# Kernel optimization log

Hardware: AMD Instinct MI355X
Metric: run time of the kernel (lower is better)

## Reference

```python
import jax, jax.numpy as jnp
import numpy as np

D, D_SEQ, D_HEAD, N_HEAD = 256, 1280, 48, 8
N_NODE, B_GRAPH, S_LEN = 2048, 8, 1024
HDH = N_HEAD * D_HEAD  # 384
SCALE = float(np.sqrt(D_HEAD))
LN_EPS = 1e-5


def setup_inputs() -> dict:
    key = jax.random.key(0)
    ks = jax.random.split(key, 12)
    node = jax.random.normal(ks[0], (N_NODE, D), dtype=jnp.float32)
    emb = jax.random.normal(ks[1], (B_GRAPH, S_LEN, D_SEQ), dtype=jnp.float32)
    mask = jax.random.randint(ks[2], (B_GRAPH, S_LEN), 0, 2, dtype=jnp.int32)
    batch = jnp.sort(jax.random.randint(ks[3], (N_NODE,), 0, B_GRAPH, dtype=jnp.int64))
    def lin(k, fan_in, fan_out):
        lim = 1.0 / np.sqrt(fan_in)
        return jax.random.uniform(k, (fan_in, fan_out), jnp.float32, -lim, lim)
    return {
        "node": node,
        "packed_sequence_emb": emb,
        "packed_sequence_mask": mask,
        "batch": batch,
        "ln_g": jnp.ones((D,), jnp.float32),
        "ln_b": jnp.zeros((D,), jnp.float32),
        "Wq": lin(ks[4], D, HDH),
        "Wk": lin(ks[5], D_SEQ, HDH),
        "Wv": lin(ks[6], D_SEQ, HDH),
        "Wg": lin(ks[7], D, HDH),
        "bg": jnp.zeros((HDH,), jnp.float32),
        "Wback": lin(ks[8], HDH, D),
        "bback": jnp.zeros((D,), jnp.float32),
    }


def _layernorm(x, g, b):
    mu = jnp.mean(x, axis=-1, keepdims=True)
    var = jnp.mean(jnp.square(x - mu), axis=-1, keepdims=True)
    return (x - mu) * jax.lax.rsqrt(var + LN_EPS) * g + b


def reference(node, packed_sequence_emb, packed_sequence_mask, batch,
              ln_g, ln_b, Wq, Wk, Wv, Wg, bg, Wback, bback):
    N = node.shape[0]
    y = _layernorm(node, ln_g, ln_b)                                   # [N, D]
    q = (y @ Wq).reshape(N, N_HEAD, D_HEAD)                            # [N, H, Dh]
    k = (packed_sequence_emb @ Wk).reshape(B_GRAPH, S_LEN, N_HEAD, D_HEAD)
    v = (packed_sequence_emb @ Wv).reshape(B_GRAPH, S_LEN, N_HEAD, D_HEAD)

    # scores[n, s, h] = <q[n,h], k[batch[n], s, h]> / sqrt(Dh)
    scores_all = jnp.einsum('nhd,bshd->nbsh', q, k) / SCALE            # [N, B, S, H]
    scores = jnp.take_along_axis(
        scores_all, batch[:, None, None, None].astype(jnp.int32), axis=1
    )[:, 0]                                                            # [N, S, H]

    # masked softmax over sequence axis (dim=1), mask broadcast over heads
    mask_f = packed_sequence_mask[batch].astype(scores.dtype)[:, :, None]  # [N, S, 1]
    s_max = jnp.max(jnp.where(mask_f > 0, scores, -jnp.inf), axis=1, keepdims=True)
    e = jnp.exp(scores - s_max) * mask_f
    w = e / (jnp.sum(e, axis=1, keepdims=True) + 1e-9)                 # [N, S, H]

    # out[n,h,d] = sum_s w[n,s,h] * v[batch[n], s, h, d]
    feat_all = jnp.einsum('nsh,bshd->nbhd', w, v)                      # [N, B, H, Dh]
    feat = jnp.take_along_axis(
        feat_all, batch[:, None, None, None].astype(jnp.int32), axis=1
    )[:, 0]                                                            # [N, H, Dh]

    gate = jax.nn.sigmoid(y @ Wg + bg).reshape(N, N_HEAD, D_HEAD)
    new = (gate * feat).reshape(N, HDH) @ Wback + bback
    return node + new
```

## Files before the change

kernel.cpp:

```cpp
#include <hip/hip_runtime.h>
#include <hip/hip_bf16.h>
#include <math.h>

#define D 256
#define D_SEQ 1280
#define D_HEAD 48
#define N_HEAD 8
#define HDH 384
#define N_NODE 2048
#define B_GRAPH 8
#define S_LEN 1024
#define LN_EPS 1e-5f
#define QSCALE (0.14433756729740643f * 1.4426950408889634f)
#define KVN 768
#define QGN 768
#define QROWS (N_NODE + 16)
#define TPG 40
#define NWL (TPG * 8)
#define PAD_T 164864

typedef unsigned short u16;
typedef __attribute__((ext_vector_type(8))) short short8;
typedef __attribute__((ext_vector_type(4))) short short4v;
typedef __attribute__((ext_vector_type(4))) unsigned short ushort4v;
typedef __attribute__((ext_vector_type(4))) float floatx4;

__device__ __forceinline__ u16 f2bf(float f) {
    unsigned int x = __float_as_uint(f);
    x += 0x7fff + ((x >> 16) & 1);
    return (u16)(x >> 16);
}

__device__ __forceinline__ void load_lds16(const u16* g, u16* lds) {
    __builtin_amdgcn_global_load_lds(
        (const __attribute__((address_space(1))) unsigned int*)g,
        (__attribute__((address_space(3))) unsigned int*)lds, 16, 0, 0);
}

__global__ __launch_bounds__(256)
void prep(const float* __restrict__ emb, u16* __restrict__ embb,
          const float* __restrict__ node, const float* __restrict__ ln_g,
          const float* __restrict__ ln_b, u16* __restrict__ yb,
          const float* __restrict__ Wk, const float* __restrict__ Wv,
          const float* __restrict__ Wq, const float* __restrict__ Wg,
          const float* __restrict__ Wback,
          u16* __restrict__ WT, u16* __restrict__ WT2, u16* __restrict__ WbT,
          const int* __restrict__ batch, int* __restrict__ ranges,
          int* __restrict__ wl, u16* __restrict__ Kp, u16* __restrict__ Qb) {
    const int bx = blockIdx.x;
    if (bx < 5120) {
        const size_t i = ((size_t)bx * 256 + threadIdx.x) * 8;
        const float4 a = *(const float4*)&emb[i];
        const float4 b = *(const float4*)&emb[i + 4];
        union { u16 u[8]; int4 v; } p;
        p.u[0]=f2bf(a.x); p.u[1]=f2bf(a.y); p.u[2]=f2bf(a.z); p.u[3]=f2bf(a.w);
        p.u[4]=f2bf(b.x); p.u[5]=f2bf(b.y); p.u[6]=f2bf(b.z); p.u[7]=f2bf(b.w);
        *(int4*)&embb[i] = p.v;
        return;
    }
    if (bx < 7168) {
        const int n = bx - 5120, t = threadIdx.x;
        float x = node[n * D + t];
        float s = x, sq = x * x;
        #pragma unroll
        for (int o = 32; o > 0; o >>= 1) {
            s  += __shfl_down(s, o);
            sq += __shfl_down(sq, o);
        }
        __shared__ float ss[4], sqs[4];
        if ((t & 63) == 0) { ss[t >> 6] = s; sqs[t >> 6] = sq; }
        __syncthreads();
        float S  = ss[0] + ss[1] + ss[2] + ss[3];
        float SQ = sqs[0] + sqs[1] + sqs[2] + sqs[3];
        float mu  = S * (1.f / D);
        float var = SQ * (1.f / D) - mu * mu;
        float inv = rsqrtf(var + LN_EPS);
        yb[n * D + t] = f2bf((x - mu) * inv * ln_g[t] + ln_b[t]);
        return;
    }
    if (bx < 8416) {
        int u = bx - 7168;
        const float* W; u16* WTo; int K, kx, ny, Ncols;
        if (u < 480)      { W = Wk;    WTo = WT;                       K = D_SEQ; Ncols = HDH; kx = u % 40; ny = u / 40; }
        else if (u < 960) { u -= 480;  W = Wv; WTo = WT + (size_t)HDH * D_SEQ; K = D_SEQ; Ncols = HDH; kx = u % 40; ny = u / 40; }
        else if (u < 1056){ u -= 960;  W = Wq; WTo = WT2;              K = D;   Ncols = HDH; kx = u % 8;  ny = u / 8; }
        else if (u < 1152){ u -= 1056; W = Wg; WTo = WT2 + (size_t)HDH * D; K = D; Ncols = HDH; kx = u % 8; ny = u / 8; }
        else              { u -= 1152; W = Wback; WTo = WbT;           K = HDH; Ncols = D;   kx = u % 12; ny = u / 12; }
        const int k0 = kx * 32, n0 = ny * 32;
        __shared__ float tile[32][33];
        const int tx = threadIdx.x & 31, ty = threadIdx.x >> 5;
        #pragma unroll
        for (int i = 0; i < 32; i += 8)
            tile[ty + i][tx] = W[(size_t)(k0 + ty + i) * Ncols + n0 + tx];
        __syncthreads();
        #pragma unroll
        for (int i = 0; i < 32; i += 8)
            WTo[(size_t)(n0 + ty + i) * K + k0 + tx] = f2bf(tile[tx][ty + i]);
        return;
    }
    if (bx == 8416) {
        int t = threadIdx.x;
        if (t <= B_GRAPH) {
            int lo = 0, hi = N_NODE;
            while (lo < hi) {
                int mid = (lo + hi) >> 1;
                if (batch[mid] < t) lo = mid + 1; else hi = mid;
            }
            ranges[t] = lo;
        }
        __syncthreads();
        if (t < B_GRAPH) {
            const int s = ranges[t];
            const int ntile = (ranges[t + 1] - s + 15) >> 4;
            for (int i = 0; i < TPG; ++i)
                wl[i * 8 + t] = (i < ntile) ? ((t << 16) | (s + i * 16)) : -1;
        }
        return;
    }
    const int t = (bx - 8417) * 256 + threadIdx.x;
    const int4 z = {0, 0, 0, 0};
    if (t < 131072) {
        const int row = t >> 1, half = t & 1;
        *(int4*)&Kp[(size_t)row * 64 + 48 + half * 8] = z;
    } else if (t < 164096) {
        const int u = t - 131072;
        const int row = u >> 1, half = u & 1;
        *(int4*)&Qb[(size_t)row * 64 + 48 + half * 8] = z;
    } else {
        const int u = t - 164096;
        const int row = u / 6, c = u - row * 6;
        const int hh = row >> 4, m = 2048 + (row & 15);
        *(int4*)&Qb[((size_t)hh * QROWS + m) * 64 + c * 8] = z;
    }
}

__global__ __launch_bounds__(256)
void kvqg_gemm(const u16* __restrict__ A, const u16* __restrict__ WT,
               u16* __restrict__ Kp, u16* __restrict__ V4,
               const u16* __restrict__ Ab, const u16* __restrict__ WT2,
               const float* __restrict__ bg, u16* __restrict__ Qb,
               float* __restrict__ gate) {
    __shared__ __align__(16) u16 As[128 * 32];
    __shared__ __align__(16) u16 Bs[128 * 32];
    const int tid = threadIdx.x;
    const int lane = tid & 63, wave = tid >> 6;
    const int wm64 = (wave >> 1) * 64, wn64 = (wave & 1) * 64;
    const int lm = lane & 15, lq = lane >> 4;

    if (blockIdx.x < 384) {
        const int glin = blockIdx.x;
        const int xcd = glin & 7, rest = glin >> 3;
        const int m0 = (xcd + 8 * (rest / 6)) * 128;
        const int n0 = (rest % 6) * 128;

        floatx4 acc[4][4] = {};

        const int srow = lane >> 2, scol = (lane & 3) * 8;
        const u16* ag  = &A[(size_t)(m0 + wave * 16 + srow) * D_SEQ + scol];
        const u16* ag2 = ag + (size_t)64 * D_SEQ;
        const u16* bgp = &WT[(size_t)(n0 + wave * 16 + srow) * D_SEQ + scol];
        const u16* bg2 = bgp + (size_t)64 * D_SEQ;
        u16* asb  = &As[wave * 512];
        u16* asb2 = &As[2048 + wave * 512];
        u16* bsb  = &Bs[wave * 512];
        u16* bsb2 = &Bs[2048 + wave * 512];

        for (int k0 = 0; k0 < D_SEQ; k0 += 32) {
            __syncthreads();
            load_lds16(ag + k0, asb);
            load_lds16(ag2 + k0, asb2);
            load_lds16(bgp + k0, bsb);
            load_lds16(bg2 + k0, bsb2);
            __syncthreads();

            short8 af[4], bfr[4];
            #pragma unroll
            for (int i = 0; i < 4; ++i)
                af[i] = *(const short8*)&As[(wm64 + i * 16 + lm) * 32 + lq * 8];
            #pragma unroll
            for (int j = 0; j < 4; ++j)
                bfr[j] = *(const short8*)&Bs[(wn64 + j * 16 + lm) * 32 + lq * 8];
            #pragma unroll
            for (int i = 0; i < 4; ++i)
                #pragma unroll
                for (int j = 0; j < 4; ++j)
                    acc[i][j] = __builtin_amdgcn_mfma_f32_16x16x32_bf16(
                        af[i], bfr[j], acc[i][j], 0, 0, 0);
        }

        #pragma unroll
        for (int i = 0; i < 4; ++i) {
            const int mrow = m0 + wm64 + i * 16 + lq * 4;
            const int bb = mrow >> 10, s = mrow & 1023;
            #pragma unroll
            for (int j = 0; j < 4; ++j) {
                const int n = n0 + wn64 + j * 16 + lm;
                if (n < HDH) {
                    const int hh = n / 48, dd = n - hh * 48;
                    u16* kp = &Kp[(((size_t)(bb * N_HEAD + hh)) * S_LEN + s) * 64 + dd];
                    kp[0]   = f2bf(acc[i][j][0]);
                    kp[64]  = f2bf(acc[i][j][1]);
                    kp[128] = f2bf(acc[i][j][2]);
                    kp[192] = f2bf(acc[i][j][3]);
                } else {
                    const int nv = n - HDH;
                    const int hh = nv / 48, dd = nv - hh * 48;
                    ushort4v pk;
                    pk[0] = f2bf(acc[i][j][0]); pk[1] = f2bf(acc[i][j][1]);
                    pk[2] = f2bf(acc[i][j][2]); pk[3] = f2bf(acc[i][j][3]);
                    *(ushort4v*)&V4[(((size_t)(bb * N_HEAD + hh)) * (S_LEN / 4) + (s >> 2)) * 192 + dd * 4] = pk;
                }
            }
        }
        return;
    }

    {
        const int u = blockIdx.x - 384;
        const int m0 = (u / 6) * 128, n0 = (u % 6) * 128;

        floatx4 acc[4][4] = {};
        const int sr = tid >> 2;
        const int sc = (tid & 3) * 8;

        for (int k0 = 0; k0 < D; k0 += 32) {
            const int4 a0 = *(const int4*)&Ab[(size_t)(m0 + sr) * D + k0 + sc];
            const int4 a1 = *(const int4*)&Ab[(size_t)(m0 + sr + 64) * D + k0 + sc];
            const int4 b0 = *(const int4*)&WT2[(size_t)(n0 + sr) * D + k0 + sc];
            const int4 b1 = *(const int4*)&WT2[(size_t)(n0 + sr + 64) * D + k0 + sc];
            __syncthreads();
            *(int4*)&As[sr * 32 + sc] = a0;
            *(int4*)&As[(sr + 64) * 32 + sc] = a1;
            *(int4*)&Bs[sr * 32 + sc] = b0;
            *(int4*)&Bs[(sr + 64) * 32 + sc] = b1;
            __syncthreads();

            short8 af[4], bfr[4];
            #pragma unroll
            for (int i = 0; i < 4; ++i)
                af[i] = *(const short8*)&As[(wm64 + i * 16 + lm) * 32 + lq * 8];
            #pragma unroll
            for (int i = 0; i < 4; ++i)
                bfr[i] = *(const short8*)&Bs[(wn64 + i * 16 + lm) * 32 + lq * 8];
            #pragma unroll
            for (int i = 0; i < 4; ++i)
                #pragma unroll
                for (int j = 0; j < 4; ++j)
                    acc[i][j] = __builtin_amdgcn_mfma_f32_16x16x32_bf16(
                        af[i], bfr[j], acc[i][j], 0, 0, 0);
        }

        #pragma unroll
        for (int i = 0; i < 4; ++i) {
            const int mb = m0 + wm64 + i * 16 + lq * 4;
            #pragma unroll
            for (int j = 0; j < 4; ++j) {
                const int n = n0 + wn64 + j * 16 + lm;
                #pragma unroll
                for (int r = 0; r < 4; ++r) {
                    const int m = mb + r;
                    const float v = acc[i][j][r];
                    if (n < HDH) {
                        const int hh = n / 48, dd = n - hh * 48;
                        Qb[((size_t)hh * QROWS + m) * 64 + dd] = f2bf(v * QSCALE);
                    } else {
                        const int ng = n - HDH;
                        gate[(size_t)m * HDH + ng] = 1.f / (1.f + __expf(-(v + bg[ng])));
                    }
                }
            }
        }
    }
}

__global__ __launch_bounds__(256)
void back_gemm(const u16* __restrict__ Ab, const u16* __restrict__ Bt,
               const float* __restrict__ bias, const float* __restrict__ resid,
               float* __restrict__ C) {
    __shared__ __align__(16) u16 As[128 * 32];
    __shared__ __align__(16) u16 Bs[128 * 32];
    const int tid = threadIdx.x;
    const int lane = tid & 63, wave = tid >> 6;
    const int wm = (wave >> 1) * 64, wn = (wave & 1) * 64;
    const int m0 = blockIdx.y * 128, n0 = blockIdx.x * 128;
    const int lm = lane & 15, lq = lane >> 4;

    floatx4 acc[4][4] = {};
    const int sr = tid >> 2;
    const int sc = (tid & 3) * 8;

    for (int k0 = 0; k0 < HDH; k0 += 32) {
        const int4 a0 = *(const int4*)&Ab[(size_t)(m0 + sr) * HDH + k0 + sc];
        const int4 a1 = *(const int4*)&Ab[(size_t)(m0 + sr + 64) * HDH + k0 + sc];
        const int4 b0 = *(const int4*)&Bt[(size_t)(n0 + sr) * HDH + k0 + sc];
        const int4 b1 = *(const int4*)&Bt[(size_t)(n0 + sr + 64) * HDH + k0 + sc];
        __syncthreads();
        *(int4*)&As[sr * 32 + sc] = a0;
        *(int4*)&As[(sr + 64) * 32 + sc] = a1;
        *(int4*)&Bs[sr * 32 + sc] = b0;
        *(int4*)&Bs[(sr + 64) * 32 + sc] = b1;
        __syncthreads();

        short8 af[4], bfr[4];
        #pragma unroll
        for (int i = 0; i < 4; ++i)
            af[i] = *(const short8*)&As[(wm + i * 16 + lm) * 32 + lq * 8];
        #pragma unroll
        for (int i = 0; i < 4; ++i)
            bfr[i] = *(const short8*)&Bs[(wn + i * 16 + lm) * 32 + lq * 8];
        #pragma unroll
        for (int i = 0; i < 4; ++i)
            #pragma unroll
            for (int j = 0; j < 4; ++j)
                acc[i][j] = __builtin_amdgcn_mfma_f32_16x16x32_bf16(
                    af[i], bfr[j], acc[i][j], 0, 0, 0);
    }

    #pragma unroll
    for (int i = 0; i < 4; ++i) {
        const int mb = m0 + wm + i * 16 + lq * 4;
        #pragma unroll
        for (int j = 0; j < 4; ++j) {
            const int n = n0 + wn + j * 16 + lm;
            #pragma unroll
            for (int r = 0; r < 4; ++r) {
                const int m = mb + r;
                C[(size_t)m * D + n] = acc[i][j][r] + bias[n] + resid[(size_t)m * D + n];
            }
        }
    }
}

struct Pref {
    short8 k0, k1;
    int4 mv;
    short4v v0, v1, v2;
};

__device__ __forceinline__ Pref ldpref(const u16* kbase, const u16* vbase,
                                       const int* mrow, int s, int lm, int lq) {
    Pref p;
    const u16* kr = &kbase[(size_t)(s + lm) * 64];
    p.k0 = *(const short8*)&kr[lq * 8];
    p.k1 = *(const short8*)&kr[32 + lq * 8];
    p.mv = *(const int4*)&mrow[s + lq * 4];
    const size_t vo = (size_t)((s >> 2) + lq) * 192;
    p.v0 = *(const short4v*)&vbase[vo];
    p.v1 = *(const short4v*)&vbase[vo + 64];
    p.v2 = *(const short4v*)&vbase[vo + 128];
    return p;
}

__global__ __launch_bounds__(256)
void attn_mfma(const u16* __restrict__ Qb, const u16* __restrict__ Kp,
               const u16* __restrict__ V4, const int* __restrict__ mask,
               const int* __restrict__ ranges, const int* __restrict__ wl,
               float* __restrict__ Pacc, float* __restrict__ Pl) {
    const int e = wl[blockIdx.x];
    if (e < 0) return;
    const int b = e >> 16, n0 = e & 0xffff;
    const int h = blockIdx.y, sp = blockIdx.z;
    const int nend = ranges[b + 1];
    const int NT = min(16, nend - n0);

    const int tid = threadIdx.x;
    const int wave = tid >> 6, lane = tid & 63;
    const int lm = lane & 15, lq = lane >> 4;
    const int bh = b * N_HEAD + h;

    const u16* qrow = &Qb[((size_t)h * QROWS + n0 + lm) * 64];
    const short8 qf0 = *(const short8*)&qrow[lq * 8];
    const short8 qf1 = *(const short8*)&qrow[32 + lq * 8];

    const u16* kbase = &Kp[(size_t)bh * S_LEN * 64];
    const u16* vbase = &V4[(size_t)bh * (S_LEN / 4) * 192 + (size_t)lm * 4];
    const int* mrow = &mask[b * S_LEN];

    float l_i = 0.f;
    floatx4 acc0 = {}, acc1 = {}, acc2 = {};

    const int sbase = sp * 512 + wave * 128;
    Pref pf[2];
    pf[0] = ldpref(kbase, vbase, mrow, sbase, lm, lq);
    pf[1] = ldpref(kbase, vbase, mrow, sbase + 16, lm, lq);

    #pragma unroll
    for (int t = 0; t < 8; ++t) {
        const Pref cur = pf[t & 1];
        if (t < 6)
            pf[t & 1] = ldpref(kbase, vbase, mrow, sbase + (t + 2) * 16, lm, lq);

        floatx4 st = {};
        st = __builtin_amdgcn_mfma_f32_16x16x32_bf16(cur.k0, qf0, st, 0, 0, 0);
        st = __builtin_amdgcn_mfma_f32_16x16x32_bf16(cur.k1, qf1, st, 0, 0, 0);

        const float p0 = cur.mv.x > 0 ? exp2f(st[0]) : 0.f;
        const float p1 = cur.mv.y > 0 ? exp2f(st[1]) : 0.f;
        const float p2 = cur.mv.z > 0 ? exp2f(st[2]) : 0.f;
        const float p3 = cur.mv.w > 0 ? exp2f(st[3]) : 0.f;
        l_i += (p0 + p1) + (p2 + p3);

        union { __hip_bfloat162 h2[2]; short4v v; } pu;
        pu.h2[0] = __float22bfloat162_rn(make_float2(p0, p1));
        pu.h2[1] = __float22bfloat162_rn(make_float2(p2, p3));

        acc0 = __builtin_amdgcn_mfma_f32_16x16x16bf16_1k(cur.v0, pu.v, acc0, 0, 0, 0);
        acc1 = __builtin_amdgcn_mfma_f32_16x16x16bf16_1k(cur.v1, pu.v, acc1, 0, 0, 0);
        acc2 = __builtin_amdgcn_mfma_f32_16x16x16bf16_1k(cur.v2, pu.v, acc2, 0, 0, 0);
    }

    l_i += __shfl_xor(l_i, 16);
    l_i += __shfl_xor(l_i, 32);

    __shared__ float sl[4][64];
    __shared__ float sacc[4][3][4][64];
    sl[wave][lane] = l_i;
    #pragma unroll
    for (int r = 0; r < 4; ++r) {
        sacc[wave][0][r][lane] = acc0[r];
        sacc[wave][1][r][lane] = acc1[r];
        sacc[wave][2][r][lane] = acc2[r];
    }
    __syncthreads();
    if (wave < 3 && lm < NT) {
        const int dt = wave;
        const float L = sl[0][lane] + sl[1][lane] + sl[2][lane] + sl[3][lane];
        const size_t o = (size_t)(n0 + lm) * HDH + h * 48 + dt * 16 + lq * 4;
        float4 ov;
        ov.x = sacc[0][dt][0][lane] + sacc[1][dt][0][lane] +
               sacc[2][dt][0][lane] + sacc[3][dt][0][lane];
        ov.y = sacc[0][dt][1][lane] + sacc[1][dt][1][lane] +
               sacc[2][dt][1][lane] + sacc[3][dt][1][lane];
        ov.z = sacc[0][dt][2][lane] + sacc[1][dt][2][lane] +
               sacc[2][dt][2][lane] + sacc[3][dt][2][lane];
        ov.w = sacc[0][dt][3][lane] + sacc[1][dt][3][lane] +
               sacc[2][dt][3][lane] + sacc[3][dt][3][lane];
        *(float4*)&Pacc[(size_t)sp * N_NODE * HDH + o] = ov;
        if (wave == 0 && lq == 0)
            Pl[(size_t)sp * N_NODE * N_HEAD + (n0 + lm) * N_HEAD + h] = L;
    }
}

__global__ __launch_bounds__(256)
void fuse_kernel(const float* __restrict__ Pacc, const float* __restrict__ Pl,
                 const float* __restrict__ gate, u16* __restrict__ gfeatb) {
    const size_t i4 = ((size_t)blockIdx.x * 256 + threadIdx.x) * 4;
    const int nh = (int)(i4 / 48);
    const float4 a = *(const float4*)&Pacc[i4];
    const float4 c = *(const float4*)&Pacc[(size_t)N_NODE * HDH + i4];
    const float4 g = *(const float4*)&gate[i4];
    const float L = Pl[nh] + Pl[N_NODE * N_HEAD + nh];
    const float inv = 1.f / (L + 1e-9f);
    union { __hip_bfloat162 h2[2]; ushort4v v; } r2;
    r2.h2[0] = __float22bfloat162_rn(make_float2((a.x + c.x) * inv * g.x,
                                                 (a.y + c.y) * inv * g.y));
    r2.h2[1] = __float22bfloat162_rn(make_float2((a.z + c.z) * inv * g.z,
                                                 (a.w + c.w) * inv * g.w));
    *(ushort4v*)&gfeatb[i4] = r2.v;
}

extern "C" void kernel_launch(void* const* d_in, const int* in_sizes, int n_in,
                              void* d_out, int out_size, void* d_ws, size_t ws_size,
                              hipStream_t stream) {
    const float* node  = (const float*)d_in[0];
    const float* emb   = (const float*)d_in[1];
    const int*   mask  = (const int*)d_in[2];
    const int*   batch = (const int*)d_in[3];
    const float* ln_g  = (const float*)d_in[4];
    const float* ln_b  = (const float*)d_in[5];
    const float* Wq    = (const float*)d_in[6];
    const float* Wk    = (const float*)d_in[7];
    const float* Wv    = (const float*)d_in[8];
    const float* Wg    = (const float*)d_in[9];
    const float* bg    = (const float*)d_in[10];
    const float* Wback = (const float*)d_in[11];
    const float* bback = (const float*)d_in[12];
    float* out = (float*)d_out;

    float* ws    = (float*)d_ws;
    float* gate  = ws;
    float* Pacc  = gate + (size_t)N_NODE * HDH;
    float* Pl    = Pacc + (size_t)2 * N_NODE * HDH;
    u16*   gfeatb = (u16*)(Pl + (size_t)2 * N_NODE * N_HEAD);
    u16*   yb    = gfeatb + (size_t)N_NODE * HDH;
    u16*   WT    = yb + (size_t)N_NODE * D;
    u16*   WT2   = WT + (size_t)KVN * D_SEQ;
    u16*   WbT   = WT2 + (size_t)QGN * D;
    u16*   Qb    = WbT + (size_t)D * HDH;
    u16*   Kp    = Qb + (size_t)N_HEAD * QROWS * 64;
    u16*   V4    = Kp + (size_t)B_GRAPH * N_HEAD * S_LEN * 64;
    u16*   embb  = V4 + (size_t)B_GRAPH * N_HEAD * (S_LEN / 4) * 192;
    int*   ranges = (int*)(embb + (size_t)B_GRAPH * S_LEN * D_SEQ);
    int*   wl    = ranges + 16;

    prep<<<8417 + PAD_T / 256, 256, 0, stream>>>(
        emb, embb, node, ln_g, ln_b, yb, Wk, Wv, Wq, Wg, Wback,
        WT, WT2, WbT, batch, ranges, wl, Kp, Qb);
    kvqg_gemm<<<480, 256, 0, stream>>>(embb, WT, Kp, V4, yb, WT2, bg, Qb, gate);
    attn_mfma<<<dim3(NWL, N_HEAD, 2), 256, 0, stream>>>(
        Qb, Kp, V4, mask, ranges, wl, Pacc, Pl);
    fuse_kernel<<<(N_NODE * HDH) / (256 * 4), 256, 0, stream>>>(
        Pacc, Pl, gate, gfeatb);
    back_gemm<<<dim3(D / 128, N_NODE / 128), 256, 0, stream>>>(
        gfeatb, WbT, bback, node, out);
}
```

Before: 186.9 us.

## Double-buffer LDS tiles with async direct-to-LDS loads in all GEMMs

```diff
diff --git a/kernel.cpp b/kernel.cpp
--- a/kernel.cpp
+++ b/kernel.cpp
@@ -140,12 +140,13 @@
                const u16* __restrict__ Ab, const u16* __restrict__ WT2,
                const float* __restrict__ bg, u16* __restrict__ Qb,
                float* __restrict__ gate) {
-    __shared__ __align__(16) u16 As[128 * 32];
-    __shared__ __align__(16) u16 Bs[128 * 32];
+    __shared__ __align__(16) u16 As[2][128 * 32];
+    __shared__ __align__(16) u16 Bs[2][128 * 32];
     const int tid = threadIdx.x;
     const int lane = tid & 63, wave = tid >> 6;
     const int wm64 = (wave >> 1) * 64, wn64 = (wave & 1) * 64;
     const int lm = lane & 15, lq = lane >> 4;
+    const int srow = lane >> 2, scol = (lane & 3) * 8;
 
     if (blockIdx.x < 384) {
         const int glin = blockIdx.x;
@@ -155,37 +156,44 @@
 
         floatx4 acc[4][4] = {};
 
-        const int srow = lane >> 2, scol = (lane & 3) * 8;
         const u16* ag  = &A[(size_t)(m0 + wave * 16 + srow) * D_SEQ + scol];
         const u16* ag2 = ag + (size_t)64 * D_SEQ;
         const u16* bgp = &WT[(size_t)(n0 + wave * 16 + srow) * D_SEQ + scol];
         const u16* bg2 = bgp + (size_t)64 * D_SEQ;
-        u16* asb  = &As[wave * 512];
-        u16* asb2 = &As[2048 + wave * 512];
-        u16* bsb  = &Bs[wave * 512];
-        u16* bsb2 = &Bs[2048 + wave * 512];
-
+        const int wo  = wave * 512;
+        const int wo2 = 2048 + wave * 512;
+
+        load_lds16(ag,  &As[0][wo]);
+        load_lds16(ag2, &As[0][wo2]);
+        load_lds16(bgp, &Bs[0][wo]);
+        load_lds16(bg2, &Bs[0][wo2]);
+        __syncthreads();
+
+        int cur = 0;
         for (int k0 = 0; k0 < D_SEQ; k0 += 32) {
-            __syncthreads();
-            load_lds16(ag + k0, asb);
-            load_lds16(ag2 + k0, asb2);
-            load_lds16(bgp + k0, bsb);
-            load_lds16(bg2 + k0, bsb2);
-            __syncthreads();
+            const int nxt = k0 + 32;
+            if (nxt < D_SEQ) {
+                load_lds16(ag  + nxt, &As[cur ^ 1][wo]);
+                load_lds16(ag2 + nxt, &As[cur ^ 1][wo2]);
+                load_lds16(bgp + nxt, &Bs[cur ^ 1][wo]);
+                load_lds16(bg2 + nxt, &Bs[cur ^ 1][wo2]);
+            }
 
             short8 af[4], bfr[4];
             #pragma unroll
             for (int i = 0; i < 4; ++i)
-                af[i] = *(const short8*)&As[(wm64 + i * 16 + lm) * 32 + lq * 8];
+                af[i] = *(const short8*)&As[cur][(wm64 + i * 16 + lm) * 32 + lq * 8];
             #pragma unroll
             for (int j = 0; j < 4; ++j)
-                bfr[j] = *(const short8*)&Bs[(wn64 + j * 16 + lm) * 32 + lq * 8];
+                bfr[j] = *(const short8*)&Bs[cur][(wn64 + j * 16 + lm) * 32 + lq * 8];
             #pragma unroll
             for (int i = 0; i < 4; ++i)
                 #pragma unroll
                 for (int j = 0; j < 4; ++j)
                     acc[i][j] = __builtin_amdgcn_mfma_f32_16x16x32_bf16(
                         af[i], bfr[j], acc[i][j], 0, 0, 0);
+            __syncthreads();
+            cur ^= 1;
         }
 
         #pragma unroll
@@ -220,34 +228,45 @@
         const int m0 = (u / 6) * 128, n0 = (u % 6) * 128;
 
         floatx4 acc[4][4] = {};
-        const int sr = tid >> 2;
-        const int sc = (tid & 3) * 8;
-
+
+        const u16* ag  = &Ab[(size_t)(m0 + wave * 16 + srow) * D + scol];
+        const u16* ag2 = ag + (size_t)64 * D;
+        const u16* bgp = &WT2[(size_t)(n0 + wave * 16 + srow) * D + scol];
+        const u16* bg2 = bgp + (size_t)64 * D;
+        const int wo  = wave * 512;
+        const int wo2 = 2048 + wave * 512;
+
+        load_lds16(ag,  &As[0][wo]);
+        load_lds16(ag2, &As[0][wo2]);
+        load_lds16(bgp, &Bs[0][wo]);
+        load_lds16(bg2, &Bs[0][wo2]);
+        __syncthreads();
+
+        int cur = 0;
         for (int k0 = 0; k0 < D; k0 += 32) {
-            const int4 a0 = *(const int4*)&Ab[(size_t)(m0 + sr) * D + k0 + sc];
-            const int4 a1 = *(const int4*)&Ab[(size_t)(m0 + sr + 64) * D + k0 + sc];
-            const int4 b0 = *(const int4*)&WT2[(size_t)(n0 + sr) * D + k0 + sc];
-            const int4 b1 = *(const int4*)&WT2[(size_t)(n0 + sr + 64) * D + k0 + sc];
-            __syncthreads();
-            *(int4*)&As[sr * 32 + sc] = a0;
-            *(int4*)&As[(sr + 64) * 32 + sc] = a1;
-            *(int4*)&Bs[sr * 32 + sc] = b0;
-            *(int4*)&Bs[(sr + 64) * 32 + sc] = b1;
-            __syncthreads();
+            const int nxt = k0 + 32;
+            if (nxt < D) {
+                load_lds16(ag  + nxt, &As[cur ^ 1][wo]);
+                load_lds16(ag2 + nxt, &As[cur ^ 1][wo2]);
+                load_lds16(bgp + nxt, &Bs[cur ^ 1][wo]);
+                load_lds16(bg2 + nxt, &Bs[cur ^ 1][wo2]);
+            }
 
             short8 af[4], bfr[4];
             #pragma unroll
             for (int i = 0; i < 4; ++i)
-                af[i] = *(const short8*)&As[(wm64 + i * 16 + lm) * 32 + lq * 8];
+                af[i] = *(const short8*)&As[cur][(wm64 + i * 16 + lm) * 32 + lq * 8];
             #pragma unroll
             for (int i = 0; i < 4; ++i)
-                bfr[i] = *(const short8*)&Bs[(wn64 + i * 16 + lm) * 32 + lq * 8];
+                bfr[i] = *(const short8*)&Bs[cur][(wn64 + i * 16 + lm) * 32 + lq * 8];
             #pragma unroll
             for (int i = 0; i < 4; ++i)
                 #pragma unroll
                 for (int j = 0; j < 4; ++j)
                     acc[i][j] = __builtin_amdgcn_mfma_f32_16x16x32_bf16(
                         af[i], bfr[j], acc[i][j], 0, 0, 0);
+            __syncthreads();
+            cur ^= 1;
         }
 
         #pragma unroll
@@ -277,43 +296,55 @@
 void back_gemm(const u16* __restrict__ Ab, const u16* __restrict__ Bt,
                const float* __restrict__ bias, const float* __restrict__ resid,
                float* __restrict__ C) {
-    __shared__ __align__(16) u16 As[128 * 32];
-    __shared__ __align__(16) u16 Bs[128 * 32];
+    __shared__ __align__(16) u16 As[2][128 * 32];
+    __shared__ __align__(16) u16 Bs[2][128 * 32];
     const int tid = threadIdx.x;
     const int lane = tid & 63, wave = tid >> 6;
     const int wm = (wave >> 1) * 64, wn = (wave & 1) * 64;
     const int m0 = blockIdx.y * 128, n0 = blockIdx.x * 128;
     const int lm = lane & 15, lq = lane >> 4;
+    const int srow = lane >> 2, scol = (lane & 3) * 8;
 
     floatx4 acc[4][4] = {};
-    const int sr = tid >> 2;
-    const int sc = (tid & 3) * 8;
-
+
+    const u16* ag  = &Ab[(size_t)(m0 + wave * 16 + srow) * HDH + scol];
+    const u16* ag2 = ag + (size_t)64 * HDH;
+    const u16* bgp = &Bt[(size_t)(n0 + wave * 16 + srow) * HDH + scol];
+    const u16* bg2 = bgp + (size_t)64 * HDH;
+    const int wo  = wave * 512;
+    const int wo2 = 2048 + wave * 512;
+
+    load_lds16(ag,  &As[0][wo]);
+    load_lds16(ag2, &As[0][wo2]);
+    load_lds16(bgp, &Bs[0][wo]);
+    load_lds16(bg2, &Bs[0][wo2]);
+    __syncthreads();
+
+    int cur = 0;
     for (int k0 = 0; k0 < HDH; k0 += 32) {
-        const int4 a0 = *(const int4*)&Ab[(size_t)(m0 + sr) * HDH + k0 + sc];
-        const int4 a1 = *(const int4*)&Ab[(size_t)(m0 + sr + 64) * HDH + k0 + sc];
-        const int4 b0 = *(const int4*)&Bt[(size_t)(n0 + sr) * HDH + k0 + sc];
-        const int4 b1 = *(const int4*)&Bt[(size_t)(n0 + sr + 64) * HDH + k0 + sc];
-        __syncthreads();
-        *(int4*)&As[sr * 32 + sc] = a0;
-        *(int4*)&As[(sr + 64) * 32 + sc] = a1;
-        *(int4*)&Bs[sr * 32 + sc] = b0;
-        *(int4*)&Bs[(sr + 64) * 32 + sc] = b1;
-        __syncthreads();
+        const int nxt = k0 + 32;
+        if (nxt < HDH) {
+            load_lds16(ag  + nxt, &As[cur ^ 1][wo]);
+            load_lds16(ag2 + nxt, &As[cur ^ 1][wo2]);
+            load_lds16(bgp + nxt, &Bs[cur ^ 1][wo]);
+            load_lds16(bg2 + nxt, &Bs[cur ^ 1][wo2]);
+        }
 
         short8 af[4], bfr[4];
         #pragma unroll
         for (int i = 0; i < 4; ++i)
-            af[i] = *(const short8*)&As[(wm + i * 16 + lm) * 32 + lq * 8];
+            af[i] = *(const short8*)&As[cur][(wm + i * 16 + lm) * 32 + lq * 8];
         #pragma unroll
         for (int i = 0; i < 4; ++i)
-            bfr[i] = *(const short8*)&Bs[(wn + i * 16 + lm) * 32 + lq * 8];
+            bfr[i] = *(const short8*)&Bs[cur][(wn + i * 16 + lm) * 32 + lq * 8];
         #pragma unroll
         for (int i = 0; i < 4; ++i)
             #pragma unroll
             for (int j = 0; j < 4; ++j)
                 acc[i][j] = __builtin_amdgcn_mfma_f32_16x16x32_bf16(
                     af[i], bfr[j], acc[i][j], 0, 0, 0);
+        __syncthreads();
+        cur ^= 1;
     }
 
     #pragma unroll
```

Measured after the change: 200.5 us. 1.07x slower.

## Compact masked sequence rows and skip masked K/V GEMM and attention work

Applied to the files above, without the earlier changes.

```diff
diff --git a/kernel.cpp b/kernel.cpp
--- a/kernel.cpp
+++ b/kernel.cpp
@@ -45,21 +45,64 @@
           const float* __restrict__ Wq, const float* __restrict__ Wg,
           const float* __restrict__ Wback,
           u16* __restrict__ WT, u16* __restrict__ WT2, u16* __restrict__ WbT,
-          const int* __restrict__ batch, int* __restrict__ ranges,
-          int* __restrict__ wl, u16* __restrict__ Kp, u16* __restrict__ Qb) {
+          const int* __restrict__ batch, const int* __restrict__ mask,
+          int* __restrict__ ranges, int* __restrict__ wl,
+          int* __restrict__ kvwl, int* __restrict__ scnt,
+          u16* __restrict__ Kp, u16* __restrict__ Qb) {
     const int bx = blockIdx.x;
-    if (bx < 5120) {
-        const size_t i = ((size_t)bx * 256 + threadIdx.x) * 8;
-        const float4 a = *(const float4*)&emb[i];
-        const float4 b = *(const float4*)&emb[i + 4];
-        union { u16 u[8]; int4 v; } p;
-        p.u[0]=f2bf(a.x); p.u[1]=f2bf(a.y); p.u[2]=f2bf(a.z); p.u[3]=f2bf(a.w);
-        p.u[4]=f2bf(b.x); p.u[5]=f2bf(b.y); p.u[6]=f2bf(b.z); p.u[7]=f2bf(b.w);
-        *(int4*)&embb[i] = p.v;
+    const int tid = threadIdx.x;
+    if (bx < 512) {
+        const int b = bx >> 6, chunk = bx & 63;
+        __shared__ unsigned long long words[16];
+        __shared__ int wpre[17];
+        #pragma unroll
+        for (int c = 0; c < 4; ++c) {
+            const int s = c * 256 + tid;
+            const unsigned long long bal = __ballot(mask[b * S_LEN + s] != 0);
+            if ((tid & 63) == 0) words[c * 4 + (tid >> 6)] = bal;
+        }
+        __syncthreads();
+        if (tid == 0) {
+            int a = 0;
+            #pragma unroll
+            for (int w = 0; w < 16; ++w) { wpre[w] = a; a += __popcll(words[w]); }
+            wpre[16] = a;
+        }
+        __syncthreads();
+        const int cnt = wpre[16];
+        const int ce = (cnt + 127) & ~127;
+        const int r = chunk * 16 + (tid >> 4);
+        const int sub = tid & 15;
+        const unsigned long long w = words[r >> 6];
+        const bool on = (w >> (r & 63)) & 1ull;
+        if (on) {
+            const int rank = wpre[r >> 6] +
+                __popcll(w & ((1ull << (r & 63)) - 1ull));
+            const float* src = &emb[((size_t)b * S_LEN + r) * D_SEQ];
+            u16* dst = &embb[((size_t)b * S_LEN + rank) * D_SEQ];
+            #pragma unroll
+            for (int it = 0; it < 10; ++it) {
+                const int off = it * 128 + sub * 8;
+                const float4 a = *(const float4*)&src[off];
+                const float4 b4 = *(const float4*)&src[off + 4];
+                union { u16 u[8]; int4 v; } p;
+                p.u[0]=f2bf(a.x); p.u[1]=f2bf(a.y); p.u[2]=f2bf(a.z); p.u[3]=f2bf(a.w);
+                p.u[4]=f2bf(b4.x); p.u[5]=f2bf(b4.y); p.u[6]=f2bf(b4.z); p.u[7]=f2bf(b4.w);
+                *(int4*)&dst[off] = p.v;
+            }
+        }
+        const int c2 = chunk * 16 + (tid >> 4);
+        if (c2 >= cnt && c2 < ce) {
+            u16* dst = &embb[((size_t)b * S_LEN + c2) * D_SEQ];
+            const int4 z = {0, 0, 0, 0};
+            #pragma unroll
+            for (int it = 0; it < 10; ++it)
+                *(int4*)&dst[it * 128 + sub * 8] = z;
+        }
         return;
     }
-    if (bx < 7168) {
-        const int n = bx - 5120, t = threadIdx.x;
+    if (bx < 2560) {
+        const int n = bx - 512, t = tid;
         float x = node[n * D + t];
         float s = x, sq = x * x;
         #pragma unroll
@@ -78,8 +121,8 @@
         yb[n * D + t] = f2bf((x - mu) * inv * ln_g[t] + ln_b[t]);
         return;
     }
-    if (bx < 8416) {
-        int u = bx - 7168;
+    if (bx < 3808) {
+        int u = bx - 2560;
         const float* W; u16* WTo; int K, kx, ny, Ncols;
         if (u < 480)      { W = Wk;    WTo = WT;                       K = D_SEQ; Ncols = HDH; kx = u % 40; ny = u / 40; }
         else if (u < 960) { u -= 480;  W = Wv; WTo = WT + (size_t)HDH * D_SEQ; K = D_SEQ; Ncols = HDH; kx = u % 40; ny = u / 40; }
@@ -88,7 +131,7 @@
         else              { u -= 1152; W = Wback; WTo = WbT;           K = HDH; Ncols = D;   kx = u % 12; ny = u / 12; }
         const int k0 = kx * 32, n0 = ny * 32;
         __shared__ float tile[32][33];
-        const int tx = threadIdx.x & 31, ty = threadIdx.x >> 5;
+        const int tx = tid & 31, ty = tid >> 5;
         #pragma unroll
         for (int i = 0; i < 32; i += 8)
             tile[ty + i][tx] = W[(size_t)(k0 + ty + i) * Ncols + n0 + tx];
@@ -98,8 +141,15 @@
             WTo[(size_t)(n0 + ty + i) * K + k0 + tx] = f2bf(tile[tx][ty + i]);
         return;
     }
-    if (bx == 8416) {
-        int t = threadIdx.x;
+    if (bx == 3808) {
+        const int t = tid;
+        __shared__ int msum[8][32];
+        __shared__ int mcnt[8];
+        const int g = t >> 5, ii = t & 31;
+        int p = 0;
+        #pragma unroll
+        for (int k = 0; k < 32; ++k) p += mask[g * S_LEN + k * 32 + ii];
+        msum[g][ii] = p;
         if (t <= B_GRAPH) {
             int lo = 0, hi = N_NODE;
             while (lo < hi) {
@@ -109,15 +159,26 @@
             ranges[t] = lo;
         }
         __syncthreads();
+        if (t < 8) {
+            int s = 0;
+            #pragma unroll
+            for (int k = 0; k < 32; ++k) s += msum[t][k];
+            mcnt[t] = s;
+            scnt[t] = s;
+        }
+        __syncthreads();
         if (t < B_GRAPH) {
             const int s = ranges[t];
             const int ntile = (ranges[t + 1] - s + 15) >> 4;
             for (int i = 0; i < TPG; ++i)
                 wl[i * 8 + t] = (i < ntile) ? ((t << 16) | (s + i * 16)) : -1;
+            const int tc = (mcnt[t] + 127) >> 7;
+            for (int i = 0; i < 8; ++i)
+                kvwl[i * 8 + t] = (i < tc) ? (t * S_LEN + i * 128) : -1;
         }
         return;
     }
-    const int t = (bx - 8417) * 256 + threadIdx.x;
+    const int t = (bx - 3809) * 256 + tid;
     const int4 z = {0, 0, 0, 0};
     if (t < 131072) {
         const int row = t >> 1, half = t & 1;
@@ -139,7 +200,7 @@
                u16* __restrict__ Kp, u16* __restrict__ V4,
                const u16* __restrict__ Ab, const u16* __restrict__ WT2,
                const float* __restrict__ bg, u16* __restrict__ Qb,
-               float* __restrict__ gate) {
+               float* __restrict__ gate, const int* __restrict__ kvwl) {
     __shared__ __align__(16) u16 As[128 * 32];
     __shared__ __align__(16) u16 Bs[128 * 32];
     const int tid = threadIdx.x;
@@ -148,10 +209,10 @@
     const int lm = lane & 15, lq = lane >> 4;
 
     if (blockIdx.x < 384) {
-        const int glin = blockIdx.x;
-        const int xcd = glin & 7, rest = glin >> 3;
-        const int m0 = (xcd + 8 * (rest / 6)) * 128;
-        const int n0 = (rest % 6) * 128;
+        const int e = kvwl[blockIdx.x / 6];
+        if (e < 0) return;
+        const int m0 = e;
+        const int n0 = (blockIdx.x % 6) * 128;
 
         floatx4 acc[4][4] = {};
 
@@ -333,17 +394,15 @@
 
 struct Pref {
     short8 k0, k1;
-    int4 mv;
     short4v v0, v1, v2;
 };
 
 __device__ __forceinline__ Pref ldpref(const u16* kbase, const u16* vbase,
-                                       const int* mrow, int s, int lm, int lq) {
+                                       int s, int lm, int lq) {
     Pref p;
     const u16* kr = &kbase[(size_t)(s + lm) * 64];
     p.k0 = *(const short8*)&kr[lq * 8];
     p.k1 = *(const short8*)&kr[32 + lq * 8];
-    p.mv = *(const int4*)&mrow[s + lq * 4];
     const size_t vo = (size_t)((s >> 2) + lq) * 192;
     p.v0 = *(const short4v*)&vbase[vo];
     p.v1 = *(const short4v*)&vbase[vo + 64];
@@ -353,7 +412,7 @@
 
 __global__ __launch_bounds__(256)
 void attn_mfma(const u16* __restrict__ Qb, const u16* __restrict__ Kp,
-               const u16* __restrict__ V4, const int* __restrict__ mask,
+               const u16* __restrict__ V4, const int* __restrict__ scnt,
                const int* __restrict__ ranges, const int* __restrict__ wl,
                float* __restrict__ Pacc, float* __restrict__ Pl) {
     const int e = wl[blockIdx.x];
@@ -374,39 +433,47 @@
 
     const u16* kbase = &Kp[(size_t)bh * S_LEN * 64];
     const u16* vbase = &V4[(size_t)bh * (S_LEN / 4) * 192 + (size_t)lm * 4];
-    const int* mrow = &mask[b * S_LEN];
+
+    const int cnt = scnt[b];
+    const int T = (cnt + 15) >> 4;
+    const int j = sp * 4 + wave;
+    const int nt = (j < T) ? (((T - 1 - j) >> 3) + 1) : 0;
 
     float l_i = 0.f;
     floatx4 acc0 = {}, acc1 = {}, acc2 = {};
 
-    const int sbase = sp * 512 + wave * 128;
-    Pref pf[2];
-    pf[0] = ldpref(kbase, vbase, mrow, sbase, lm, lq);
-    pf[1] = ldpref(kbase, vbase, mrow, sbase + 16, lm, lq);
-
-    #pragma unroll
-    for (int t = 0; t < 8; ++t) {
-        const Pref cur = pf[t & 1];
-        if (t < 6)
-            pf[t & 1] = ldpref(kbase, vbase, mrow, sbase + (t + 2) * 16, lm, lq);
-
+    Pref pA, pB;
+    if (nt > 0) pA = ldpref(kbase, vbase, j * 16, lm, lq);
+    if (nt > 1) pB = ldpref(kbase, vbase, (j + 8) * 16, lm, lq);
+
+    int t = 0;
+    auto step = [&](Pref& P) {
+        const int s0 = (j + t * 8) * 16;
         floatx4 st = {};
-        st = __builtin_amdgcn_mfma_f32_16x16x32_bf16(cur.k0, qf0, st, 0, 0, 0);
-        st = __builtin_amdgcn_mfma_f32_16x16x32_bf16(cur.k1, qf1, st, 0, 0, 0);
-
-        const float p0 = cur.mv.x > 0 ? exp2f(st[0]) : 0.f;
-        const float p1 = cur.mv.y > 0 ? exp2f(st[1]) : 0.f;
-        const float p2 = cur.mv.z > 0 ? exp2f(st[2]) : 0.f;
-        const float p3 = cur.mv.w > 0 ? exp2f(st[3]) : 0.f;
+        st = __builtin_amdgcn_mfma_f32_16x16x32_bf16(P.k0, qf0, st, 0, 0, 0);
+        st = __builtin_amdgcn_mfma_f32_16x16x32_bf16(P.k1, qf1, st, 0, 0, 0);
+        const short4v v0 = P.v0, v1 = P.v1, v2 = P.v2;
+        if (t + 2 < nt) P = ldpref(kbase, vbase, (j + (t + 2) * 8) * 16, lm, lq);
+
+        const int rem = cnt - s0 - lq * 4;
+        const float p0 = rem > 0 ? exp2f(st[0]) : 0.f;
+        const float p1 = rem > 1 ? exp2f(st[1]) : 0.f;
+        const float p2 = rem > 2 ? exp2f(st[2]) : 0.f;
+        const float p3 = rem > 3 ? exp2f(st[3]) : 0.f;
         l_i += (p0 + p1) + (p2 + p3);
 
         union { __hip_bfloat162 h2[2]; short4v v; } pu;
         pu.h2[0] = __float22bfloat162_rn(make_float2(p0, p1));
         pu.h2[1] = __float22bfloat162_rn(make_float2(p2, p3));
 
-        acc0 = __builtin_amdgcn_mfma_f32_16x16x16bf16_1k(cur.v0, pu.v, acc0, 0, 0, 0);
-        acc1 = __builtin_amdgcn_mfma_f32_16x16x16bf16_1k(cur.v1, pu.v, acc1, 0, 0, 0);
-        acc2 = __builtin_amdgcn_mfma_f32_16x16x16bf16_1k(cur.v2, pu.v, acc2, 0, 0, 0);
+        acc0 = __builtin_amdgcn_mfma_f32_16x16x16bf16_1k(v0, pu.v, acc0, 0, 0, 0);
+        acc1 = __builtin_amdgcn_mfma_f32_16x16x16bf16_1k(v1, pu.v, acc1, 0, 0, 0);
+        acc2 = __builtin_amdgcn_mfma_f32_16x16x16bf16_1k(v2, pu.v, acc2, 0, 0, 0);
+        ++t;
+    };
+    while (t < nt) {
+        step(pA);
+        if (t < nt) step(pB);
     }
 
     l_i += __shfl_xor(l_i, 16);
@@ -492,13 +559,15 @@
     u16*   embb  = V4 + (size_t)B_GRAPH * N_HEAD * (S_LEN / 4) * 192;
     int*   ranges = (int*)(embb + (size_t)B_GRAPH * S_LEN * D_SEQ);
     int*   wl    = ranges + 16;
-
-    prep<<<8417 + PAD_T / 256, 256, 0, stream>>>(
+    int*   kvwl  = wl + NWL;
+    int*   scnt  = kvwl + 64;
+
+    prep<<<3809 + PAD_T / 256, 256, 0, stream>>>(
         emb, embb, node, ln_g, ln_b, yb, Wk, Wv, Wq, Wg, Wback,
-        WT, WT2, WbT, batch, ranges, wl, Kp, Qb);
-    kvqg_gemm<<<480, 256, 0, stream>>>(embb, WT, Kp, V4, yb, WT2, bg, Qb, gate);
+        WT, WT2, WbT, batch, mask, ranges, wl, kvwl, scnt, Kp, Qb);
+    kvqg_gemm<<<480, 256, 0, stream>>>(embb, WT, Kp, V4, yb, WT2, bg, Qb, gate, kvwl);
     attn_mfma<<<dim3(NWL, N_HEAD, 2), 256, 0, stream>>>(
-        Qb, Kp, V4, mask, ranges, wl, Pacc, Pl);
+        Qb, Kp, V4, scnt, ranges, wl, Pacc, Pl);
     fuse_kernel<<<(N_NODE * HDH) / (256 * 4), 256, 0, stream>>>(
         Pacc, Pl, gate, gfeatb);
     back_gemm<<<dim3(D / 128, N_NODE / 128), 256, 0, stream>>>(
```

Measured after the change: 176.1 us. 1.06x faster.
